# Kernel optimization log

Hardware: AMD Instinct MI355X
Metric: run time of the kernel (lower is better)

The kernel has to match this reference:

```python
import math
import jax, jax.numpy as jnp
import numpy as np

B, S, E, H, DK, NW = 2048, 1, 1024, 128, 8, 8  # d_k == n_wires == 8, seq_len must be 1
DIM = 2 ** NW


def setup_inputs() -> dict:
    key = jax.random.key(0)
    ks = jax.random.split(key, 7)
    scale = 1.0 / math.sqrt(E)
    return {
        "x": jax.random.normal(ks[0], (B, S, E), jnp.float32),
        "wq": jax.random.normal(ks[1], (E, E), jnp.float32) * scale,
        "wk": jax.random.normal(ks[2], (E, E), jnp.float32) * scale,
        "wv": jax.random.normal(ks[3], (E, E), jnp.float32) * scale,
        "wc": jax.random.normal(ks[4], (E, E), jnp.float32) * scale,
        "bc": jax.random.normal(ks[5], (E,), jnp.float32) * 0.01,
        "rx_params": jax.random.normal(ks[6], (NW,), jnp.float32),  # trainable RX angles (shared q_layer)
    }


def _apply_rx(state, theta, wire):
    # state: (N, 2,...,2) [NW qubit axes]; theta: scalar or (N,)
    N = state.shape[0]
    theta = jnp.broadcast_to(theta, (N,))
    c = jnp.cos(theta * 0.5).astype(jnp.complex64)[:, None]
    s = (-1j * jnp.sin(theta * 0.5).astype(jnp.complex64))[:, None]
    st = jnp.moveaxis(state, wire + 1, 1).reshape(N, 2, -1)
    new = jnp.stack([c * st[:, 0] + s * st[:, 1],
                     s * st[:, 0] + c * st[:, 1]], axis=1)
    return jnp.moveaxis(new.reshape((N,) + (2,) * NW), 1, wire + 1)


def _apply_cnot(state, ctrl, tgt):
    st = jnp.moveaxis(state, (ctrl + 1, tgt + 1), (1, 2))
    st = jnp.stack([st[:, 0], jnp.flip(st[:, 1], axis=1)], axis=1)
    return jnp.moveaxis(st, (1, 2), (ctrl + 1, tgt + 1))


def _qlayer(angles, rx_params):
    # angles: (N, NW) per-sample RX encoder angles; rx_params: (NW,) shared trainable RX
    N = angles.shape[0]
    state = jnp.zeros((N,) + (2,) * NW, jnp.complex64)
    state = state.at[(slice(None),) + (0,) * NW].set(1.0 + 0j)  # |0...0>
    for w in range(NW):
        state = _apply_rx(state, angles[:, w], w)      # encoder RX(x_w)
    for w in range(NW):
        state = _apply_rx(state, rx_params[w], w)      # trainable RX
    for w in range(NW - 1):
        state = _apply_cnot(state, w, w + 1)           # CNOT chain
    state = _apply_cnot(state, NW - 1, 0)              # ring closure
    probs = jnp.abs(state.reshape(N, DIM)) ** 2
    bits = (jnp.arange(DIM)[:, None] >> jnp.arange(NW - 1, -1, -1)[None, :]) & 1  # wire 0 = MSB
    signs = (1.0 - 2.0 * bits).astype(jnp.float32)     # (DIM, NW)
    return probs @ signs                               # <Z_w> per wire, (N, NW)


def reference(x, wq, wk, wv, wc, bc, rx_params):
    q = jnp.einsum('bse,fe->bsf', x, wq).reshape(B, S, H, DK)
    k = jnp.einsum('bse,fe->bsf', x, wk).reshape(B, S, H, DK)
    v = jnp.einsum('bse,fe->bsf', x, wv).reshape(B, S, H, DK)
    scores = jnp.einsum('bqhd,bkhd->bhqk', q, k) / math.sqrt(DK)
    attn = jax.nn.softmax(scores, axis=-1)             # dropout is identity in eval
    out = jnp.einsum('bhqk,bkhd->bqhd', attn, v).reshape(B, S, E)
    # per-head quantum circuit (S==1, d_k==NW); batch all heads together
    angles = out.reshape(B * H, DK)
    qout = _qlayer(angles, rx_params).reshape(B, S, E)
    return jnp.einsum('bse,fe->bsf', qout, wc) + bc
```

## Files before the change

### kernel.cpp

```cpp
#include <hip/hip_runtime.h>
#include <hip/hip_bf16.h>
#include <math.h>


#define BB 2048
#define EN 1024

typedef short s16x8 __attribute__((ext_vector_type(8)));
typedef float f32x4 __attribute__((ext_vector_type(4)));

union Frag { s16x8 v; __hip_bfloat16 h[8]; };

__device__ inline s16x8 cvt_frag(f32x4 lo, f32x4 hi) {
    Frag u;
    #pragma unroll
    for (int j = 0; j < 4; ++j) {
        u.h[j]     = __float2bfloat16(lo[j]);
        u.h[4 + j] = __float2bfloat16(hi[j]);
    }
    return u.v;
}

__device__ inline void gll16(const __hip_bfloat16* g, __hip_bfloat16* l) {
    __builtin_amdgcn_global_load_lds(
        (const __attribute__((address_space(1))) void*)g,
        (__attribute__((address_space(3))) void*)l,
        16, 0, 0);
}

__global__ __launch_bounds__(256) void cvt3_kernel(
        const float* __restrict__ x, const float* __restrict__ wv,
        const float* __restrict__ wc,
        __hip_bfloat16* __restrict__ xb, __hip_bfloat16* __restrict__ wvb,
        __hip_bfloat16* __restrict__ wcb)
{
    const int g = blockIdx.x * 256 + threadIdx.x;
    const int NX = (BB * EN) / 8;
    const int NG = (EN * EN) / 8;
    const float* s; __hip_bfloat16* d; size_t off;
    if (g < NX)           { s = x;  d = xb;  off = (size_t)g * 8; }
    else if (g < NX + NG) { s = wv; d = wvb; off = (size_t)(g - NX) * 8; }
    else                  { s = wc; d = wcb; off = (size_t)(g - NX - NG) * 8; }
    f32x4 lo = *(const f32x4*)(s + off);
    f32x4 hi = *(const f32x4*)(s + off + 4);
    *(s16x8*)(d + off) = cvt_frag(lo, hi);
}

template <int EPI>
__global__ __launch_bounds__(512, 4) void gemm_kernel(
        const __hip_bfloat16* __restrict__ A,
        const __hip_bfloat16* __restrict__ W,
        const float* __restrict__ bias, const float* __restrict__ rx,
        void* __restrict__ Cv)
{
    __shared__ __align__(16) unsigned char smem[32768];
    __hip_bfloat16* lds = (__hip_bfloat16*)smem;

    const int tid  = threadIdx.x;
    const int wave = tid >> 6, lane = tid & 63;
    const int l15 = lane & 15, lq = lane >> 4;
    const int m0 = blockIdx.x * 64, n0 = blockIdx.y * 64;
    const int wmt = wave >> 1;
    const int wnt = wave & 1;

    const __hip_bfloat16* gsrc[2];
    int ldst[2];
    #pragma unroll
    for (int i = 0; i < 2; ++i) {
        const int t = wave * 2 + i;
        int row, lofs;
        const __hip_bfloat16* base;
        if (t < 8) { const int mt = t >> 1; row = m0 + mt * 16 + l15; base = A; lofs = t * 512; }
        else       { const int u = t - 8;   row = n0 + (u >> 1) * 16 + l15; base = W; lofs = 4096 + u * 512; }
        gsrc[i] = base + (size_t)row * EN + (t & 1) * 32 + lq * 8;
        ldst[i] = lofs;
    }

    f32x4 acc[2] = {};

    #pragma unroll
    for (int i = 0; i < 2; ++i) gll16(gsrc[i], &lds[ldst[i]]);
    __syncthreads();

    int p = 0;
    for (int k0 = 64; k0 <= EN; k0 += 64) {
        if (k0 < EN) {
            const int q = p ^ 1;
            #pragma unroll
            for (int i = 0; i < 2; ++i) gll16(gsrc[i] + k0, &lds[q * 8192 + ldst[i]]);
        }
        const __hip_bfloat16* Ab = &lds[p * 8192];
        const __hip_bfloat16* Bb = Ab + 4096;
        #pragma unroll
        for (int kt = 0; kt < 2; ++kt) {
            s16x8 a = *(const s16x8*)&Ab[(wmt * 2 + kt) * 512 + lane * 8];
            #pragma unroll
            for (int j = 0; j < 2; ++j) {
                s16x8 b = *(const s16x8*)&Bb[((wnt * 2 + j) * 2 + kt) * 512 + lane * 8];
                acc[j] = __builtin_amdgcn_mfma_f32_16x16x32_bf16(a, b, acc[j], 0, 0, 0);
            }
        }
        __syncthreads();
        p ^= 1;
    }

    if (EPI == 0) {
        float* sb = (float*)smem;
        #pragma unroll
        for (int j = 0; j < 2; ++j) {
            const int col = wnt * 32 + j * 16 + l15;
            #pragma unroll
            for (int r = 0; r < 4; ++r)
                sb[(wmt * 16 + lq * 4 + r) * 68 + col] = acc[j][r];
        }
        __syncthreads();
        const int row = tid >> 3, g = tid & 7;
        const float* pv = &sb[row * 68 + g * 8];
        float t[8];
        #pragma unroll
        for (int j = 0; j < 8; ++j) t[j] = __cosf(pv[j] + rx[j]);
        Frag o;
        float suf = t[1];
        #pragma unroll
        for (int j = 2; j < 8; ++j) suf *= t[j];
        o.h[0] = __float2bfloat16(suf);
        float pr = t[0];
        #pragma unroll
        for (int j = 1; j < 8; ++j) { pr *= t[j]; o.h[j] = __float2bfloat16(pr); }
        __hip_bfloat16* V = (__hip_bfloat16*)Cv;
        *(s16x8*)(V + (size_t)(m0 + row) * EN + n0 + g * 8) = o.v;
    } else {
        float* C = (float*)Cv;
        #pragma unroll
        for (int j = 0; j < 2; ++j) {
            const int col = n0 + wnt * 32 + j * 16 + l15;
            const float bv = bias[col];
            #pragma unroll
            for (int r = 0; r < 4; ++r) {
                const int row = m0 + wmt * 16 + lq * 4 + r;
                C[(size_t)row * EN + col] = acc[j][r] + bv;
            }
        }
    }
}

extern "C" void kernel_launch(void* const* d_in, const int* in_sizes, int n_in,
                              void* d_out, int out_size, void* d_ws, size_t ws_size,
                              hipStream_t stream)
{
    const float* x  = (const float*)d_in[0];
    const float* wv = (const float*)d_in[3];
    const float* wc = (const float*)d_in[4];
    const float* bc = (const float*)d_in[5];
    const float* rx = (const float*)d_in[6];
    float* out = (float*)d_out;

    const size_t XE = (size_t)BB * EN;
    const size_t WE = (size_t)EN * EN;

    __hip_bfloat16* xb  = (__hip_bfloat16*)d_ws;
    __hip_bfloat16* wvb = xb + XE;
    __hip_bfloat16* wcb = wvb + WE;
    __hip_bfloat16* V   = wcb + WE;

    dim3 grid(BB / 64, EN / 64);
    cvt3_kernel<<<(int)((XE / 8 + 2 * (WE / 8)) / 256), 256, 0, stream>>>(
        x, wv, wc, xb, wvb, wcb);
    gemm_kernel<0><<<grid, 512, 0, stream>>>(xb, wvb, nullptr, rx, V);
    gemm_kernel<1><<<grid, 512, 0, stream>>>(V, wcb, bc, nullptr, out);
}
```

Measured before the change: 113.0 us.

## Split K across wave groups with 32x32 wave tiles and LDS reduction

Reorganizes the eight waves of each GEMM block into two K-halves. Each half computes a 32x32 output sub-tile using one of the two 32-wide K slices of every 64-wide K step, where before each wave computed a 16x32 tile over the full step. This cuts LDS fragment reads per MFMA from six loads per four MFMAs to four. The cost is an extra LDS reduction of partial accumulators at the end, one extra barrier, more accumulator registers and slightly more shared memory.

Result: no change. 113.9 us (+0.8%).

```diff
diff --git a/kernel.cpp b/kernel.cpp
--- a/kernel.cpp
+++ b/kernel.cpp
@@ -53,15 +53,17 @@
         const float* __restrict__ bias, const float* __restrict__ rx,
         void* __restrict__ Cv)
 {
-    __shared__ __align__(16) unsigned char smem[32768];
+    __shared__ __align__(16) unsigned char smem[33792];
     __hip_bfloat16* lds = (__hip_bfloat16*)smem;
 
     const int tid  = threadIdx.x;
     const int wave = tid >> 6, lane = tid & 63;
     const int l15 = lane & 15, lq = lane >> 4;
     const int m0 = blockIdx.x * 64, n0 = blockIdx.y * 64;
-    const int wmt = wave >> 1;
-    const int wnt = wave & 1;
+    const int wk  = wave >> 2;
+    const int wmn = wave & 3;
+    const int wm  = wmn >> 1;
+    const int wn  = wmn & 1;
 
     const __hip_bfloat16* gsrc[2];
     int ldst[2];
@@ -76,7 +78,7 @@
         ldst[i] = lofs;
     }
 
-    f32x4 acc[2] = {};
+    f32x4 acc[2][2] = {};
 
     #pragma unroll
     for (int i = 0; i < 2; ++i) gll16(gsrc[i], &lds[ldst[i]]);
@@ -91,27 +93,49 @@
         }
         const __hip_bfloat16* Ab = &lds[p * 8192];
         const __hip_bfloat16* Bb = Ab + 4096;
-        #pragma unroll
-        for (int kt = 0; kt < 2; ++kt) {
-            s16x8 a = *(const s16x8*)&Ab[(wmt * 2 + kt) * 512 + lane * 8];
-            #pragma unroll
-            for (int j = 0; j < 2; ++j) {
-                s16x8 b = *(const s16x8*)&Bb[((wnt * 2 + j) * 2 + kt) * 512 + lane * 8];
-                acc[j] = __builtin_amdgcn_mfma_f32_16x16x32_bf16(a, b, acc[j], 0, 0, 0);
-            }
+        s16x8 a[2], b[2];
+        #pragma unroll
+        for (int mi = 0; mi < 2; ++mi)
+            a[mi] = *(const s16x8*)&Ab[((wm * 2 + mi) * 2 + wk) * 512 + lane * 8];
+        #pragma unroll
+        for (int nj = 0; nj < 2; ++nj)
+            b[nj] = *(const s16x8*)&Bb[((wn * 2 + nj) * 2 + wk) * 512 + lane * 8];
+        #pragma unroll
+        for (int mi = 0; mi < 2; ++mi) {
+            #pragma unroll
+            for (int nj = 0; nj < 2; ++nj)
+                acc[mi][nj] = __builtin_amdgcn_mfma_f32_16x16x32_bf16(
+                    a[mi], b[nj], acc[mi][nj], 0, 0, 0);
         }
         __syncthreads();
         p ^= 1;
     }
 
+    float* red = (float*)(smem + 17408);
+    if (wk == 1) {
+        #pragma unroll
+        for (int mi = 0; mi < 2; ++mi) {
+            #pragma unroll
+            for (int nj = 0; nj < 2; ++nj)
+                *(f32x4*)&red[((wmn * 2 + mi) * 2 + nj) * 256 + lane * 4] = acc[mi][nj];
+        }
+    }
+    __syncthreads();
+
     if (EPI == 0) {
         float* sb = (float*)smem;
-        #pragma unroll
-        for (int j = 0; j < 2; ++j) {
-            const int col = wnt * 32 + j * 16 + l15;
-            #pragma unroll
-            for (int r = 0; r < 4; ++r)
-                sb[(wmt * 16 + lq * 4 + r) * 68 + col] = acc[j][r];
+        if (wk == 0) {
+            #pragma unroll
+            for (int mi = 0; mi < 2; ++mi) {
+                #pragma unroll
+                for (int nj = 0; nj < 2; ++nj) {
+                    f32x4 o = *(const f32x4*)&red[((wmn * 2 + mi) * 2 + nj) * 256 + lane * 4];
+                    const int col = wn * 32 + nj * 16 + l15;
+                    #pragma unroll
+                    for (int r = 0; r < 4; ++r)
+                        sb[(wm * 32 + mi * 16 + lq * 4 + r) * 68 + col] = acc[mi][nj][r] + o[r];
+                }
+            }
         }
         __syncthreads();
         const int row = tid >> 3, g = tid & 7;
@@ -130,15 +154,21 @@
         __hip_bfloat16* V = (__hip_bfloat16*)Cv;
         *(s16x8*)(V + (size_t)(m0 + row) * EN + n0 + g * 8) = o.v;
     } else {
-        float* C = (float*)Cv;
-        #pragma unroll
-        for (int j = 0; j < 2; ++j) {
-            const int col = n0 + wnt * 32 + j * 16 + l15;
-            const float bv = bias[col];
-            #pragma unroll
-            for (int r = 0; r < 4; ++r) {
-                const int row = m0 + wmt * 16 + lq * 4 + r;
-                C[(size_t)row * EN + col] = acc[j][r] + bv;
+        if (wk == 0) {
+            float* C = (float*)Cv;
+            #pragma unroll
+            for (int mi = 0; mi < 2; ++mi) {
+                #pragma unroll
+                for (int nj = 0; nj < 2; ++nj) {
+                    f32x4 o = *(const f32x4*)&red[((wmn * 2 + mi) * 2 + nj) * 256 + lane * 4];
+                    const int col = n0 + wn * 32 + nj * 16 + l15;
+                    const float bv = bias[col];
+                    #pragma unroll
+                    for (int r = 0; r < 4; ++r) {
+                        const int row = m0 + wm * 32 + mi * 16 + lq * 4 + r;
+                        C[(size_t)row * EN + col] = acc[mi][nj][r] + o[r] + bv;
+                    }
+                }
             }
         }
     }
```

## Fuse conversion and both GEMMs into one cooperative kernel with grid syncs

Applied to the files above, without the earlier changes.

Replaces the three launches (fp32-to-bf16 conversion, V GEMM with cosine-product epilogue, output GEMM with bias) with a single cooperative kernel of 512 blocks. Grid-wide barriers separate the stages. The aim is to remove per-launch overhead and the gaps between kernels. In exchange, all 512 blocks must be co-resident, and each grid sync costs a device-wide barrier.

Measured after the change: 233.1 us. +106.2%, slower.

```diff
diff --git a/kernel.cpp b/kernel.cpp
--- a/kernel.cpp
+++ b/kernel.cpp
@@ -1,4 +1,5 @@
 #include <hip/hip_runtime.h>
+#include <hip/hip_cooperative_groups.h>
 #include <hip/hip_bf16.h>
 #include <math.h>
 
@@ -28,38 +29,13 @@
         16, 0, 0);
 }
 
-__global__ __launch_bounds__(256) void cvt3_kernel(
-        const float* __restrict__ x, const float* __restrict__ wv,
-        const float* __restrict__ wc,
-        __hip_bfloat16* __restrict__ xb, __hip_bfloat16* __restrict__ wvb,
-        __hip_bfloat16* __restrict__ wcb)
-{
-    const int g = blockIdx.x * 256 + threadIdx.x;
-    const int NX = (BB * EN) / 8;
-    const int NG = (EN * EN) / 8;
-    const float* s; __hip_bfloat16* d; size_t off;
-    if (g < NX)           { s = x;  d = xb;  off = (size_t)g * 8; }
-    else if (g < NX + NG) { s = wv; d = wvb; off = (size_t)(g - NX) * 8; }
-    else                  { s = wc; d = wcb; off = (size_t)(g - NX - NG) * 8; }
-    f32x4 lo = *(const f32x4*)(s + off);
-    f32x4 hi = *(const f32x4*)(s + off + 4);
-    *(s16x8*)(d + off) = cvt_frag(lo, hi);
-}
-
-template <int EPI>
-__global__ __launch_bounds__(512, 4) void gemm_kernel(
+__device__ __forceinline__ void gemm64(
         const __hip_bfloat16* __restrict__ A,
         const __hip_bfloat16* __restrict__ W,
-        const float* __restrict__ bias, const float* __restrict__ rx,
-        void* __restrict__ Cv)
+        __hip_bfloat16* lds, int m0, int n0, int tid, f32x4* acc)
 {
-    __shared__ __align__(16) unsigned char smem[32768];
-    __hip_bfloat16* lds = (__hip_bfloat16*)smem;
-
-    const int tid  = threadIdx.x;
     const int wave = tid >> 6, lane = tid & 63;
     const int l15 = lane & 15, lq = lane >> 4;
-    const int m0 = blockIdx.x * 64, n0 = blockIdx.y * 64;
     const int wmt = wave >> 1;
     const int wnt = wave & 1;
 
@@ -75,8 +51,6 @@
         gsrc[i] = base + (size_t)row * EN + (t & 1) * 32 + lq * 8;
         ldst[i] = lofs;
     }
-
-    f32x4 acc[2] = {};
 
     #pragma unroll
     for (int i = 0; i < 2; ++i) gll16(gsrc[i], &lds[ldst[i]]);
@@ -103,8 +77,51 @@
         __syncthreads();
         p ^= 1;
     }
+}
 
-    if (EPI == 0) {
+__global__ __launch_bounds__(512, 4) void mega_kernel(
+        const float* __restrict__ x,  const float* __restrict__ wv,
+        const float* __restrict__ wc, const float* __restrict__ bc,
+        const float* __restrict__ rx,
+        __hip_bfloat16* __restrict__ xb, __hip_bfloat16* __restrict__ wvb,
+        __hip_bfloat16* __restrict__ wcb,
+        __hip_bfloat16* __restrict__ V, float* __restrict__ out)
+{
+    __shared__ __align__(16) unsigned char smem[33792];
+    __hip_bfloat16* lds = (__hip_bfloat16*)smem;
+
+    const int tid = threadIdx.x;
+    const int bid = blockIdx.x;
+
+    {
+        const int NG = (EN * EN) / 8;
+        const int gt = bid * 512 + tid;
+        {
+            f32x4 lo = *(const f32x4*)(x + (size_t)gt * 8);
+            f32x4 hi = *(const f32x4*)(x + (size_t)gt * 8 + 4);
+            *(s16x8*)(xb + (size_t)gt * 8) = cvt_frag(lo, hi);
+        }
+        {
+            const float* s; __hip_bfloat16* d; size_t off;
+            if (gt < NG) { s = wv; d = wvb; off = (size_t)gt * 8; }
+            else         { s = wc; d = wcb; off = (size_t)(gt - NG) * 8; }
+            f32x4 lo = *(const f32x4*)(s + off);
+            f32x4 hi = *(const f32x4*)(s + off + 4);
+            *(s16x8*)(d + off) = cvt_frag(lo, hi);
+        }
+    }
+    cooperative_groups::this_grid().sync();
+
+    const int bx = bid & 31, by = bid >> 5;
+    const int m0 = bx * 64, n0 = by * 64;
+    const int wave = tid >> 6, lane = tid & 63;
+    const int l15 = lane & 15, lq = lane >> 4;
+    const int wmt = wave >> 1, wnt = wave & 1;
+
+    {
+        f32x4 acc[2] = {};
+        gemm64(xb, wvb, lds, m0, n0, tid, acc);
+
         float* sb = (float*)smem;
         #pragma unroll
         for (int j = 0; j < 2; ++j) {
@@ -127,18 +144,22 @@
         float pr = t[0];
         #pragma unroll
         for (int j = 1; j < 8; ++j) { pr *= t[j]; o.h[j] = __float2bfloat16(pr); }
-        __hip_bfloat16* V = (__hip_bfloat16*)Cv;
         *(s16x8*)(V + (size_t)(m0 + row) * EN + n0 + g * 8) = o.v;
-    } else {
-        float* C = (float*)Cv;
+    }
+    cooperative_groups::this_grid().sync();
+
+    {
+        f32x4 acc[2] = {};
+        gemm64(V, wcb, lds, m0, n0, tid, acc);
+
         #pragma unroll
         for (int j = 0; j < 2; ++j) {
             const int col = n0 + wnt * 32 + j * 16 + l15;
-            const float bv = bias[col];
+            const float bv = bc[col];
             #pragma unroll
             for (int r = 0; r < 4; ++r) {
                 const int row = m0 + wmt * 16 + lq * 4 + r;
-                C[(size_t)row * EN + col] = acc[j][r] + bv;
+                out[(size_t)row * EN + col] = acc[j][r] + bv;
             }
         }
     }
@@ -163,9 +184,7 @@
     __hip_bfloat16* wcb = wvb + WE;
     __hip_bfloat16* V   = wcb + WE;
 
-    dim3 grid(BB / 64, EN / 64);
-    cvt3_kernel<<<(int)((XE / 8 + 2 * (WE / 8)) / 256), 256, 0, stream>>>(
-        x, wv, wc, xb, wvb, wcb);
-    gemm_kernel<0><<<grid, 512, 0, stream>>>(xb, wvb, nullptr, rx, V);
-    gemm_kernel<1><<<grid, 512, 0, stream>>>(V, wcb, bc, nullptr, out);
+    void* args[] = { (void*)&x, (void*)&wv, (void*)&wc, (void*)&bc, (void*)&rx,
+                     (void*)&xb, (void*)&wvb, (void*)&wcb, (void*)&V, (void*)&out };
+    hipLaunchCooperativeKernel(mega_kernel, dim3(512), dim3(512), args, 0, stream);
 }
```
